# Performance work log

Measured on AMD Instinct MI355X. Metric: run time of the kernel, lower is better.

## Reference

```python
import jax, jax.numpy as jnp
import numpy as np

BS, N, C = 16, 128, 512
EPS = 1e-5


def setup_inputs() -> dict:
    key = jax.random.key(0)
    ks = jax.random.split(key, 6)
    x = jax.random.normal(ks[0], (BS, N, C), dtype=jnp.float32)
    y = jax.random.normal(ks[1], (BS, C), dtype=jnp.float32)
    # edge conv: Conv2d(2C -> 1, 1x1), init std sqrt(2/(1*1*1))
    conv_e_w = jax.random.normal(ks[2], (1, 2 * C), dtype=jnp.float32) * np.sqrt(2.0)
    conv_e_b = jnp.zeros((1,), dtype=jnp.float32)
    bn_e_g = jnp.ones((1,), dtype=jnp.float32)
    bn_e_b = jnp.zeros((1,), dtype=jnp.float32)
    bn_e_m = jnp.zeros((1,), dtype=jnp.float32)
    bn_e_v = jnp.ones((1,), dtype=jnp.float32)
    # feature conv: Conv2d(2C -> C, 1x1), init std sqrt(2/C)
    conv_f_w = jax.random.normal(ks[3], (C, 2 * C), dtype=jnp.float32) * np.sqrt(2.0 / C)
    conv_f_b = jnp.zeros((C,), dtype=jnp.float32)
    bn_f_g = jnp.ones((C,), dtype=jnp.float32)
    bn_f_b = jnp.zeros((C,), dtype=jnp.float32)
    bn_f_m = jnp.zeros((C,), dtype=jnp.float32)
    bn_f_v = jnp.ones((C,), dtype=jnp.float32)
    return {
        "x": x, "y": y,
        "conv_e_w": conv_e_w, "conv_e_b": conv_e_b,
        "bn_e_g": bn_e_g, "bn_e_b": bn_e_b, "bn_e_m": bn_e_m, "bn_e_v": bn_e_v,
        "conv_f_w": conv_f_w, "conv_f_b": conv_f_b,
        "bn_f_g": bn_f_g, "bn_f_b": bn_f_b, "bn_f_m": bn_f_m, "bn_f_v": bn_f_v,
    }


def reference(x, y, conv_e_w, conv_e_b, bn_e_g, bn_e_b, bn_e_m, bn_e_v,
              conv_f_w, conv_f_b, bn_f_g, bn_f_b, bn_f_m, bn_f_v):
    bs, n, c = x.shape
    # ---- Wcompute: pairwise |x_i - x_j| -> conv1x1(2C->1) + BN + mask + softmax ----
    diff = jnp.abs(x[:, :, None, :] - x[:, None, :, :])  # [bs, N, N, C]
    w_diff = conv_e_w[0, :c]   # weights on pairwise-diff channels
    w_y = conv_e_w[0, c:]      # weights on broadcast y channels
    # 1x1 conv collapses to einsum; y part is constant over (i, j)
    score = (jnp.einsum('bijc,c->bij', diff, w_diff)
             + (y @ w_y)[:, None, None] + conv_e_b[0])  # [bs, N, N]
    # BatchNorm2d(1), inference mode
    score = (score - bn_e_m[0]) * (bn_e_g[0] * jax.lax.rsqrt(bn_e_v[0] + EPS)) + bn_e_b[0]
    # mask diagonal (W_id * 1e8) then softmax over neighbors j
    score = score - jnp.eye(n, dtype=score.dtype)[None] * 1e8
    W = jax.nn.softmax(score, axis=2)  # [bs, N, N]
    # ---- Gconv: neighbor aggregation + conv1x1(2C->C) + BN + ReLU ----
    x_nb = jnp.einsum('bij,bjc->bic', W, x)       # [bs, N, C]
    h = jnp.concatenate([x, x_nb], axis=2)        # [bs, N, 2C]
    out = jnp.einsum('bnk,ck->bnc', h, conv_f_w) + conv_f_b  # [bs, N, C]
    # BatchNorm2d(C), inference mode (per-channel)
    out = (out - bn_f_m) * (bn_f_g * jax.lax.rsqrt(bn_f_v + EPS)) + bn_f_b
    return jax.nn.relu(out)
```

## Files before the change

### kernel.cpp

```cpp
#include <hip/hip_runtime.h>
#include <hip/hip_bf16.h>

#define NTOK 128
#define CHN  512
#define KTOT 1024
#define EPSV 1e-5f
#define LR1  129

typedef __attribute__((ext_vector_type(8))) short bf16x8;
typedef __attribute__((ext_vector_type(4))) float f32x4;

union BfPack4 { ushort4 u; __hip_bfloat16 h[4]; };

__global__ __launch_bounds__(256, 3)
void k1_score_softmax_xnb(const float* __restrict__ xg,
                          const float* __restrict__ wde,
                          const float* __restrict__ bn_e_g,
                          const float* __restrict__ bn_e_v,
                          const float* __restrict__ wf,
                          __hip_bfloat16* __restrict__ hb,
                          __hip_bfloat16* __restrict__ wfb)
{
    __shared__ float xs[64 * LR1];
    __shared__ float part1[2][4][128];
    __shared__ float wrow[4][128];
    __shared__ float red[16];

    const int t   = threadIdx.x;
    const int blk = blockIdx.x;
    const int b   = blk >> 5;
    const int i0  = (blk & 31) << 2;
    const float* __restrict__ xb = xg + (size_t)b * NTOK * CHN;

    {
        const float* wr = wf + (size_t)blk * KTOT;
        float4 u = *(const float4*)&wr[t * 4];
        BfPack4 p;
        p.h[0] = __float2bfloat16(u.x); p.h[1] = __float2bfloat16(u.y);
        p.h[2] = __float2bfloat16(u.z); p.h[3] = __float2bfloat16(u.w);
        *(ushort4*)&wfb[(size_t)blk * KTOT + t * 4] = p.u;
    }

    const int j = t & 127;
    const int q = __builtin_amdgcn_readfirstlane(t >> 7);
    float acc[4] = {0.f, 0.f, 0.f, 0.f};

    const int cl_s = (t & 15) * 4;
    const int j0_s = t >> 4;

    for (int s = 0; s < 8; ++s) {
        const int cs = s * 64;
        #pragma unroll
        for (int u = 0; u < 8; ++u) {
            const int jj = j0_s + 16 * u;
            float4 v = *(const float4*)&xb[(size_t)jj * CHN + cs + cl_s];
            xs[(cl_s + 0) * LR1 + jj] = v.x;
            xs[(cl_s + 1) * LR1 + jj] = v.y;
            xs[(cl_s + 2) * LR1 + jj] = v.z;
            xs[(cl_s + 3) * LR1 + jj] = v.w;
        }
        __syncthreads();

        const int cb = cs + q * 32;
        #pragma unroll
        for (int g = 0; g < 8; ++g) {
            const int c = cb + g * 4;
            const float4 wd  = *(const float4*)&wde[c];
            const float4 xi0 = *(const float4*)&xb[(size_t)(i0 + 0) * CHN + c];
            const float4 xi1 = *(const float4*)&xb[(size_t)(i0 + 1) * CHN + c];
            const float4 xi2 = *(const float4*)&xb[(size_t)(i0 + 2) * CHN + c];
            const float4 xi3 = *(const float4*)&xb[(size_t)(i0 + 3) * CHN + c];
            const float* xr = &xs[(q * 32 + g * 4) * LR1 + j];
            const float xj0 = xr[0 * LR1];
            const float xj1 = xr[1 * LR1];
            const float xj2 = xr[2 * LR1];
            const float xj3 = xr[3 * LR1];
            acc[0] += fabsf(xi0.x - xj0) * wd.x + fabsf(xi0.y - xj1) * wd.y
                    + fabsf(xi0.z - xj2) * wd.z + fabsf(xi0.w - xj3) * wd.w;
            acc[1] += fabsf(xi1.x - xj0) * wd.x + fabsf(xi1.y - xj1) * wd.y
                    + fabsf(xi1.z - xj2) * wd.z + fabsf(xi1.w - xj3) * wd.w;
            acc[2] += fabsf(xi2.x - xj0) * wd.x + fabsf(xi2.y - xj1) * wd.y
                    + fabsf(xi2.z - xj2) * wd.z + fabsf(xi2.w - xj3) * wd.w;
            acc[3] += fabsf(xi3.x - xj0) * wd.x + fabsf(xi3.y - xj1) * wd.y
                    + fabsf(xi3.z - xj2) * wd.z + fabsf(xi3.w - xj3) * wd.w;
        }
        __syncthreads();
    }

    part1[q][0][j] = acc[0];
    part1[q][1][j] = acc[1];
    part1[q][2][j] = acc[2];
    part1[q][3][j] = acc[3];
    __syncthreads();

    if (t < 128) {
        const float sc = bn_e_g[0] * rsqrtf(bn_e_v[0] + EPSV);
        float logit[4];
        #pragma unroll
        for (int ti = 0; ti < 4; ++ti) {
            logit[ti] = (part1[0][ti][t] + part1[1][ti][t]) * sc;
            if (t == i0 + ti) logit[ti] -= 1e8f;
        }
        const int wid = t >> 6, lane = t & 63;
        float mx[4];
        #pragma unroll
        for (int ti = 0; ti < 4; ++ti) {
            float v = logit[ti];
            #pragma unroll
            for (int off = 32; off > 0; off >>= 1) v = fmaxf(v, __shfl_xor(v, off));
            mx[ti] = v;
        }
        if (lane == 0) {
            red[wid * 8 + 0] = mx[0]; red[wid * 8 + 1] = mx[1];
            red[wid * 8 + 2] = mx[2]; red[wid * 8 + 3] = mx[3];
        }
        __syncthreads();
        float pe[4], sm[4];
        #pragma unroll
        for (int ti = 0; ti < 4; ++ti) {
            const float M = fmaxf(red[ti], red[8 + ti]);
            pe[ti] = __expf(logit[ti] - M);
            float v = pe[ti];
            #pragma unroll
            for (int off = 32; off > 0; off >>= 1) v += __shfl_xor(v, off);
            sm[ti] = v;
        }
        if (lane == 0) {
            red[wid * 8 + 4] = sm[0]; red[wid * 8 + 5] = sm[1];
            red[wid * 8 + 6] = sm[2]; red[wid * 8 + 7] = sm[3];
        }
        __syncthreads();
        #pragma unroll
        for (int ti = 0; ti < 4; ++ti) {
            const float S = red[4 + ti] + red[12 + ti];
            wrow[ti][t] = pe[ti] / S;
        }
    } else {
        __syncthreads();
        __syncthreads();
    }
    __syncthreads();

    float* part2 = xs;
    const int jq  = __builtin_amdgcn_readfirstlane(t >> 7);
    const int c4f = (t & 127) * 4;
    float4 a2[4];
    #pragma unroll
    for (int r = 0; r < 4; ++r) { a2[r].x = a2[r].y = a2[r].z = a2[r].w = 0.f; }

    #pragma unroll 4
    for (int jj = 0; jj < 64; ++jj) {
        const int jx = jq * 64 + jj;
        const float4 xj = *(const float4*)&xb[(size_t)jx * CHN + c4f];
        const float w0 = wrow[0][jx], w1 = wrow[1][jx];
        const float w2 = wrow[2][jx], w3 = wrow[3][jx];
        a2[0].x += w0 * xj.x; a2[0].y += w0 * xj.y; a2[0].z += w0 * xj.z; a2[0].w += w0 * xj.w;
        a2[1].x += w1 * xj.x; a2[1].y += w1 * xj.y; a2[1].z += w1 * xj.z; a2[1].w += w1 * xj.w;
        a2[2].x += w2 * xj.x; a2[2].y += w2 * xj.y; a2[2].z += w2 * xj.z; a2[2].w += w2 * xj.w;
        a2[3].x += w3 * xj.x; a2[3].y += w3 * xj.y; a2[3].z += w3 * xj.z; a2[3].w += w3 * xj.w;
    }
    #pragma unroll
    for (int r = 0; r < 4; ++r)
        *(float4*)&part2[(jq * 4 + r) * CHN + c4f] = a2[r];
    __syncthreads();

    {
        const int row = t >> 6;
        const int cc  = (t & 63) * 8;
        float4 p0a = *(const float4*)&part2[(0 + row) * CHN + cc];
        float4 p1a = *(const float4*)&part2[(4 + row) * CHN + cc];
        float4 p0b = *(const float4*)&part2[(0 + row) * CHN + cc + 4];
        float4 p1b = *(const float4*)&part2[(4 + row) * CHN + cc + 4];
        const size_t rowg = (size_t)(b * NTOK + i0 + row);
        BfPack4 pa, pb;
        pa.h[0] = __float2bfloat16(p0a.x + p1a.x);
        pa.h[1] = __float2bfloat16(p0a.y + p1a.y);
        pa.h[2] = __float2bfloat16(p0a.z + p1a.z);
        pa.h[3] = __float2bfloat16(p0a.w + p1a.w);
        pb.h[0] = __float2bfloat16(p0b.x + p1b.x);
        pb.h[1] = __float2bfloat16(p0b.y + p1b.y);
        pb.h[2] = __float2bfloat16(p0b.z + p1b.z);
        pb.h[3] = __float2bfloat16(p0b.w + p1b.w);
        *(ushort4*)&hb[rowg * KTOT + CHN + cc]     = pa.u;
        *(ushort4*)&hb[rowg * KTOT + CHN + cc + 4] = pb.u;

        const float4 xv0 = *(const float4*)&xb[(size_t)(i0 + row) * CHN + cc];
        const float4 xv1 = *(const float4*)&xb[(size_t)(i0 + row) * CHN + cc + 4];
        pa.h[0] = __float2bfloat16(xv0.x); pa.h[1] = __float2bfloat16(xv0.y);
        pa.h[2] = __float2bfloat16(xv0.z); pa.h[3] = __float2bfloat16(xv0.w);
        pb.h[0] = __float2bfloat16(xv1.x); pb.h[1] = __float2bfloat16(xv1.y);
        pb.h[2] = __float2bfloat16(xv1.z); pb.h[3] = __float2bfloat16(xv1.w);
        *(ushort4*)&hb[rowg * KTOT + cc]     = pa.u;
        *(ushort4*)&hb[rowg * KTOT + cc + 4] = pb.u;
    }
}

__global__ __launch_bounds__(256)
void k2_gemm_bn_relu(const __hip_bfloat16* __restrict__ hbp,
                     const __hip_bfloat16* __restrict__ wfbp,
                     const float* __restrict__ fb,
                     const float* __restrict__ gg,
                     const float* __restrict__ bb,
                     const float* __restrict__ mm,
                     const float* __restrict__ vv,
                     float* __restrict__ out)
{
    const int blk  = blockIdx.x;
    const int r0   = (blk >> 3) << 6;
    const int c0   = (blk & 7) << 6;
    const int t    = threadIdx.x;
    const int w    = t >> 6;
    const int lane = t & 63;
    const int wm   = w & 1;
    const int wn   = w >> 1;
    const int m16  = lane & 15;
    const int qq   = lane >> 4;

    const short* A0 = (const short*)hbp  + (size_t)(r0 + wm * 32 + m16) * KTOT + qq * 8;
    const short* B0 = (const short*)wfbp + (size_t)(c0 + wn * 32 + m16) * KTOT + qq * 8;

    f32x4 acc00 = {0.f, 0.f, 0.f, 0.f};
    f32x4 acc01 = acc00, acc10 = acc00, acc11 = acc00;

    #pragma unroll 4
    for (int k0 = 0; k0 < KTOT; k0 += 32) {
        const bf16x8 aA = *(const bf16x8*)(A0 + k0);
        const bf16x8 aB = *(const bf16x8*)(A0 + 16 * KTOT + k0);
        const bf16x8 bA = *(const bf16x8*)(B0 + k0);
        const bf16x8 bB = *(const bf16x8*)(B0 + 16 * KTOT + k0);
        acc00 = __builtin_amdgcn_mfma_f32_16x16x32_bf16(aA, bA, acc00, 0, 0, 0);
        acc01 = __builtin_amdgcn_mfma_f32_16x16x32_bf16(aA, bB, acc01, 0, 0, 0);
        acc10 = __builtin_amdgcn_mfma_f32_16x16x32_bf16(aB, bA, acc10, 0, 0, 0);
        acc11 = __builtin_amdgcn_mfma_f32_16x16x32_bf16(aB, bB, acc11, 0, 0, 0);
    }

    #pragma unroll
    for (int ni = 0; ni < 2; ++ni) {
        const int c = c0 + wn * 32 + ni * 16 + m16;
        const float gf = gg[c] * rsqrtf(vv[c] + EPSV);
        const float ad = fb[c] - mm[c];
        const float bv = bb[c];
        const f32x4 acr0 = ni ? acc01 : acc00;
        const f32x4 acr1 = ni ? acc11 : acc10;
        #pragma unroll
        for (int r2 = 0; r2 < 4; ++r2) {
            int row = r0 + wm * 32 + qq * 4 + r2;
            float val = (acr0[r2] + ad) * gf + bv;
            out[(size_t)row * CHN + c] = fmaxf(val, 0.f);
            row += 16;
            val = (acr1[r2] + ad) * gf + bv;
            out[(size_t)row * CHN + c] = fmaxf(val, 0.f);
        }
    }
}

extern "C" void kernel_launch(void* const* d_in, const int* in_sizes, int n_in,
                              void* d_out, int out_size, void* d_ws, size_t ws_size,
                              hipStream_t stream) {
    const float* x        = (const float*)d_in[0];
    const float* conv_e_w = (const float*)d_in[2];
    const float* bn_e_g   = (const float*)d_in[4];
    const float* bn_e_v   = (const float*)d_in[7];
    const float* conv_f_w = (const float*)d_in[8];
    const float* conv_f_b = (const float*)d_in[9];
    const float* bn_f_g   = (const float*)d_in[10];
    const float* bn_f_b   = (const float*)d_in[11];
    const float* bn_f_m   = (const float*)d_in[12];
    const float* bn_f_v   = (const float*)d_in[13];
    float* out = (float*)d_out;

    __hip_bfloat16* hb  = (__hip_bfloat16*)d_ws;
    __hip_bfloat16* wfb = hb + (size_t)2048 * 1024;

    k1_score_softmax_xnb<<<512, 256, 0, stream>>>(x, conv_e_w, bn_e_g, bn_e_v,
                                                  conv_f_w, hb, wfb);
    k2_gemm_bn_relu<<<256, 256, 0, stream>>>(hb, wfb, conv_f_b, bn_f_g, bn_f_b,
                                             bn_f_m, bn_f_v, out);
}
```

Measured before the change: 131.9 us.

## Use XOR-swizzled float4 LDS tile and 4-way channel split in score kernel

Replaces the padded scalar transposed LDS tile with a float4 layout indexed by an XOR swizzle, so the j-side operands are read as vector loads and each thread handles two j values across a quarter of the channels. The channel-partial reduction becomes 4-way, reusing the tile buffer so the separate part1 array is gone. LDS use per block shrinks, and launch bounds are raised to four blocks per CU for more occupancy. The softmax barriers are restructured so all threads hit the same syncthreads calls. Higher occupancy may force register pressure or spills, and the 4-way partial sum adds some LDS traffic.

```diff
diff --git a/kernel.cpp b/kernel.cpp
--- a/kernel.cpp
+++ b/kernel.cpp
@@ -5,14 +5,13 @@
 #define CHN  512
 #define KTOT 1024
 #define EPSV 1e-5f
-#define LR1  129
 
 typedef __attribute__((ext_vector_type(8))) short bf16x8;
 typedef __attribute__((ext_vector_type(4))) float f32x4;
 
 union BfPack4 { ushort4 u; __hip_bfloat16 h[4]; };
 
-__global__ __launch_bounds__(256, 3)
+__global__ __launch_bounds__(256, 4)
 void k1_score_softmax_xnb(const float* __restrict__ xg,
                           const float* __restrict__ wde,
                           const float* __restrict__ bn_e_g,
@@ -21,10 +20,10 @@
                           __hip_bfloat16* __restrict__ hb,
                           __hip_bfloat16* __restrict__ wfb)
 {
-    __shared__ float xs[64 * LR1];
-    __shared__ float part1[2][4][128];
-    __shared__ float wrow[4][128];
-    __shared__ float red[16];
+    __shared__ float4 xs4[16 * 128];
+    __shared__ float  wrow[4][128];
+    __shared__ float  red[16];
+    float* pf = (float*)xs4;
 
     const int t   = threadIdx.x;
     const int blk = blockIdx.x;
@@ -41,107 +40,91 @@
         *(ushort4*)&wfb[(size_t)blk * KTOT + t * 4] = p.u;
     }
 
-    const int j = t & 127;
-    const int q = __builtin_amdgcn_readfirstlane(t >> 7);
-    float acc[4] = {0.f, 0.f, 0.f, 0.f};
-
-    const int cl_s = (t & 15) * 4;
-    const int j0_s = t >> 4;
+    const int j0 = t & 63;
+    const int q  = __builtin_amdgcn_readfirstlane(t >> 6);
+    const int c4s = t & 15;
+    const int jbs = t >> 4;
+
+    float acc[4][2] = {{0.f,0.f},{0.f,0.f},{0.f,0.f},{0.f,0.f}};
 
     for (int s = 0; s < 8; ++s) {
         const int cs = s * 64;
         #pragma unroll
         for (int u = 0; u < 8; ++u) {
-            const int jj = j0_s + 16 * u;
-            float4 v = *(const float4*)&xb[(size_t)jj * CHN + cs + cl_s];
-            xs[(cl_s + 0) * LR1 + jj] = v.x;
-            xs[(cl_s + 1) * LR1 + jj] = v.y;
-            xs[(cl_s + 2) * LR1 + jj] = v.z;
-            xs[(cl_s + 3) * LR1 + jj] = v.w;
+            const int j = jbs + 16 * u;
+            float4 v = *(const float4*)&xb[(size_t)j * CHN + cs + c4s * 4];
+            xs4[c4s * 128 + (j ^ c4s)] = v;
         }
         __syncthreads();
 
-        const int cb = cs + q * 32;
-        #pragma unroll
-        for (int g = 0; g < 8; ++g) {
-            const int c = cb + g * 4;
+        #pragma unroll
+        for (int g = 0; g < 4; ++g) {
+            const int c4r = q * 4 + g;
+            const int c   = cs + c4r * 4;
+            const int sl  = c4r * 128 + (j0 ^ c4r);
             const float4 wd  = *(const float4*)&wde[c];
-            const float4 xi0 = *(const float4*)&xb[(size_t)(i0 + 0) * CHN + c];
-            const float4 xi1 = *(const float4*)&xb[(size_t)(i0 + 1) * CHN + c];
-            const float4 xi2 = *(const float4*)&xb[(size_t)(i0 + 2) * CHN + c];
-            const float4 xi3 = *(const float4*)&xb[(size_t)(i0 + 3) * CHN + c];
-            const float* xr = &xs[(q * 32 + g * 4) * LR1 + j];
-            const float xj0 = xr[0 * LR1];
-            const float xj1 = xr[1 * LR1];
-            const float xj2 = xr[2 * LR1];
-            const float xj3 = xr[3 * LR1];
-            acc[0] += fabsf(xi0.x - xj0) * wd.x + fabsf(xi0.y - xj1) * wd.y
-                    + fabsf(xi0.z - xj2) * wd.z + fabsf(xi0.w - xj3) * wd.w;
-            acc[1] += fabsf(xi1.x - xj0) * wd.x + fabsf(xi1.y - xj1) * wd.y
-                    + fabsf(xi1.z - xj2) * wd.z + fabsf(xi1.w - xj3) * wd.w;
-            acc[2] += fabsf(xi2.x - xj0) * wd.x + fabsf(xi2.y - xj1) * wd.y
-                    + fabsf(xi2.z - xj2) * wd.z + fabsf(xi2.w - xj3) * wd.w;
-            acc[3] += fabsf(xi3.x - xj0) * wd.x + fabsf(xi3.y - xj1) * wd.y
-                    + fabsf(xi3.z - xj2) * wd.z + fabsf(xi3.w - xj3) * wd.w;
+            const float4 xja = xs4[sl];
+            const float4 xjb = xs4[sl + 64];
+            #pragma unroll
+            for (int r = 0; r < 4; ++r) {
+                const float4 xi = *(const float4*)&xb[(size_t)(i0 + r) * CHN + c];
+                acc[r][0] += fabsf(xi.x - xja.x) * wd.x + fabsf(xi.y - xja.y) * wd.y
+                           + fabsf(xi.z - xja.z) * wd.z + fabsf(xi.w - xja.w) * wd.w;
+                acc[r][1] += fabsf(xi.x - xjb.x) * wd.x + fabsf(xi.y - xjb.y) * wd.y
+                           + fabsf(xi.z - xjb.z) * wd.z + fabsf(xi.w - xjb.w) * wd.w;
+            }
         }
         __syncthreads();
     }
 
-    part1[q][0][j] = acc[0];
-    part1[q][1][j] = acc[1];
-    part1[q][2][j] = acc[2];
-    part1[q][3][j] = acc[3];
-    __syncthreads();
-
-    if (t < 128) {
+    #pragma unroll
+    for (int r = 0; r < 4; ++r) {
+        pf[q * 512 + r * 128 + j0]      = acc[r][0];
+        pf[q * 512 + r * 128 + j0 + 64] = acc[r][1];
+    }
+    __syncthreads();
+
+    const bool act = (t < 128);
+    const int wid = t >> 6, lane = t & 63;
+    float logit[4], pe[4];
+    if (act) {
         const float sc = bn_e_g[0] * rsqrtf(bn_e_v[0] + EPSV);
-        float logit[4];
-        #pragma unroll
-        for (int ti = 0; ti < 4; ++ti) {
-            logit[ti] = (part1[0][ti][t] + part1[1][ti][t]) * sc;
-            if (t == i0 + ti) logit[ti] -= 1e8f;
-        }
-        const int wid = t >> 6, lane = t & 63;
-        float mx[4];
-        #pragma unroll
-        for (int ti = 0; ti < 4; ++ti) {
-            float v = logit[ti];
+        #pragma unroll
+        for (int r = 0; r < 4; ++r) {
+            logit[r] = (pf[0 * 512 + r * 128 + t] + pf[1 * 512 + r * 128 + t]
+                      + pf[2 * 512 + r * 128 + t] + pf[3 * 512 + r * 128 + t]) * sc;
+            if (t == i0 + r) logit[r] -= 1e8f;
+        }
+        #pragma unroll
+        for (int r = 0; r < 4; ++r) {
+            float v = logit[r];
             #pragma unroll
             for (int off = 32; off > 0; off >>= 1) v = fmaxf(v, __shfl_xor(v, off));
-            mx[ti] = v;
-        }
-        if (lane == 0) {
-            red[wid * 8 + 0] = mx[0]; red[wid * 8 + 1] = mx[1];
-            red[wid * 8 + 2] = mx[2]; red[wid * 8 + 3] = mx[3];
-        }
-        __syncthreads();
-        float pe[4], sm[4];
-        #pragma unroll
-        for (int ti = 0; ti < 4; ++ti) {
-            const float M = fmaxf(red[ti], red[8 + ti]);
-            pe[ti] = __expf(logit[ti] - M);
-            float v = pe[ti];
+            if (lane == 0) red[wid * 8 + r] = v;
+        }
+    }
+    __syncthreads();
+    if (act) {
+        #pragma unroll
+        for (int r = 0; r < 4; ++r) {
+            const float M = fmaxf(red[r], red[8 + r]);
+            pe[r] = __expf(logit[r] - M);
+            float v = pe[r];
             #pragma unroll
             for (int off = 32; off > 0; off >>= 1) v += __shfl_xor(v, off);
-            sm[ti] = v;
-        }
-        if (lane == 0) {
-            red[wid * 8 + 4] = sm[0]; red[wid * 8 + 5] = sm[1];
-            red[wid * 8 + 6] = sm[2]; red[wid * 8 + 7] = sm[3];
-        }
-        __syncthreads();
-        #pragma unroll
-        for (int ti = 0; ti < 4; ++ti) {
-            const float S = red[4 + ti] + red[12 + ti];
-            wrow[ti][t] = pe[ti] / S;
-        }
-    } else {
-        __syncthreads();
-        __syncthreads();
-    }
-    __syncthreads();
-
-    float* part2 = xs;
+            if (lane == 0) red[wid * 8 + 4 + r] = v;
+        }
+    }
+    __syncthreads();
+    if (act) {
+        #pragma unroll
+        for (int r = 0; r < 4; ++r) {
+            const float S = red[4 + r] + red[12 + r];
+            wrow[r][t] = pe[r] / S;
+        }
+    }
+    __syncthreads();
+
     const int jq  = __builtin_amdgcn_readfirstlane(t >> 7);
     const int c4f = (t & 127) * 4;
     float4 a2[4];
@@ -161,16 +144,16 @@
     }
     #pragma unroll
     for (int r = 0; r < 4; ++r)
-        *(float4*)&part2[(jq * 4 + r) * CHN + c4f] = a2[r];
+        *(float4*)&pf[(jq * 4 + r) * CHN + c4f] = a2[r];
     __syncthreads();
 
     {
         const int row = t >> 6;
         const int cc  = (t & 63) * 8;
-        float4 p0a = *(const float4*)&part2[(0 + row) * CHN + cc];
-        float4 p1a = *(const float4*)&part2[(4 + row) * CHN + cc];
-        float4 p0b = *(const float4*)&part2[(0 + row) * CHN + cc + 4];
-        float4 p1b = *(const float4*)&part2[(4 + row) * CHN + cc + 4];
+        float4 p0a = *(const float4*)&pf[(0 + row) * CHN + cc];
+        float4 p1a = *(const float4*)&pf[(4 + row) * CHN + cc];
+        float4 p0b = *(const float4*)&pf[(0 + row) * CHN + cc + 4];
+        float4 p1b = *(const float4*)&pf[(4 + row) * CHN + cc + 4];
         const size_t rowg = (size_t)(b * NTOK + i0 + row);
         BfPack4 pa, pb;
         pa.h[0] = __float2bfloat16(p0a.x + p1a.x);
```

Measured after the change: 140.0 us. 6.1% more time.
